# Kernel tuning notes

Measured on AMD Instinct MI355X. Metric: run time of the kernel, lower is better.

Reference implementation:

```python
import jax, jax.numpy as jnp
import numpy as np

NUM_TAGS = 32            # init arg
N = NUM_TAGS + 2         # internal num_tags (start/end appended)
START = N - 2
END = N - 1
B = 1024
T = 1024
NEG = -6969.0            # module's 'minus infinity' constant


def setup_inputs() -> dict:
    key = jax.random.key(0)
    k1, k2 = jax.random.split(key)
    features = jax.random.normal(k1, (B, T, N), dtype=jnp.float32)
    # learned parameter: transition matrix [N, N]
    transitions = jax.random.normal(k2, (N, N), dtype=jnp.float32)
    return {"features": features, "transitions": transitions}


def _viterbi(features, transitions):
    # features: [B, T, N]; transitions: [N, N]
    Bn, Tn, Nn = features.shape
    init = jnp.full((Bn, Nn), NEG, dtype=features.dtype).at[:, START].set(0.0)

    def step(scores, feat):
        # score[b, j, k] = scores[b, k] + feat[b, j] + transitions[j, k]
        sc = scores[:, None, :] + feat[:, :, None] + transitions[None, :, :]
        return jnp.max(sc, axis=-1), jnp.argmax(sc, axis=-1)

    feats_t = jnp.swapaxes(features, 0, 1)            # [T, B, N]
    scores, paths = jax.lax.scan(step, init, feats_t)  # paths: [T, B, N] int

    scores = scores + transitions[END]                # add transition to end tag
    best = jnp.max(scores, axis=-1)                   # [B]
    idx = jnp.argmax(scores, axis=-1)                 # [B]

    # backtrack through backpointers, from t = T-1 down to 0
    def back(i, path):
        ni = jnp.take_along_axis(path, i[:, None], axis=1)[:, 0]
        return ni, ni

    _, tags = jax.lax.scan(back, idx, paths, reverse=True)  # tags: [T, B]
    best_path = jnp.concatenate([tags.T, idx[:, None]], axis=1)  # [B, T+1]
    return best, best_path


def reference(features, transitions):
    return _viterbi(features, transitions)
```

## Files before the change

### kernel.cpp

```cpp
#include <hip/hip_runtime.h>
#include <stdint.h>

#define BB 1024
#define TT 1024
#define NN 34
#define NP 36
#define CH 9
#define NB 4
#define TPB (NB * NN * 4)
#define NEGV -6969.0f
#define PADV -1.0e30f

template<int C>
__device__ __forceinline__ int dpp_i(int x) {
    return __builtin_amdgcn_update_dpp(0, x, C, 0xF, 0xF, true);
}
template<int C>
__device__ __forceinline__ float dpp_f(float x) {
    return __int_as_float(dpp_i<C>(__float_as_int(x)));
}

__global__ __launch_bounds__(TPB) void viterbi_fwd(
        const float* __restrict__ feat,
        const float* __restrict__ trans,
        unsigned char* __restrict__ bp,
        float* __restrict__ sfin)
{
    __shared__ float s_lds[2][NB * NP];

    const int tid = threadIdx.x;
    const int bl  = tid / 136;
    const int r   = tid % 136;
    const int j   = r >> 2;
    const int h   = r & 3;
    const int bg  = blockIdx.x * NB + bl;
    const int k0  = h * CH;

    float tr[CH];
#pragma unroll
    for (int i = 0; i < CH; ++i) {
        int k = k0 + i;
        tr[i] = (k < NN) ? trans[j * NN + k] : 0.0f;
    }

    for (int e = tid; e < 2 * NB * NP; e += TPB) {
        int kk = e % NP;
        float v = (kk >= NN) ? PADV : ((kk == 32) ? 0.0f : NEGV);
        s_lds[0][0] = s_lds[0][0];
        ((float*)s_lds)[e] = v;
    }

    const float* fptr = feat + (size_t)bg * TT * NN + j;
    float f = fptr[0];

    unsigned char* bprow = bp + (size_t)bg * TT * NN + j;

    __syncthreads();

    int cur = 0;
    for (int t = 0; t < TT; ++t) {
        const float* sb = &s_lds[cur][bl * NP + k0];
        float sv[CH];
#pragma unroll
        for (int i = 0; i < CH; ++i) sv[i] = sb[i];

        float fn = fptr[(size_t)((t + 1 < TT) ? t + 1 : t) * NN];

        float m = -3.0e38f;
        int am = k0;
#pragma unroll
        for (int i = 0; i < CH; ++i) {
            float v = (sv[i] + f) + tr[i];
            bool gt = v > m;
            am = gt ? (k0 + i) : am;
            m  = gt ? v : m;
        }

        {
            float vo = dpp_f<0xB1>(m);
            int   ko = dpp_i<0xB1>(am);
            bool take = (vo > m) || (vo == m && ko < am);
            m  = take ? vo : m;
            am = take ? ko : am;
            vo = dpp_f<0x4E>(m);
            ko = dpp_i<0x4E>(am);
            take = (vo > m) || (vo == m && ko < am);
            m  = take ? vo : m;
            am = take ? ko : am;
        }

        int nxt = cur ^ 1;
        if (h == 0) {
            s_lds[nxt][bl * NP + j] = m;
            bprow[(size_t)t * NN] = (unsigned char)am;
        }
        f = fn;
        cur = nxt;
        __syncthreads();
    }

    if (h == 0) sfin[bg * NN + j] = s_lds[cur][bl * NP + j];
}

__global__ __launch_bounds__(TPB) void viterbi_btk(
        const unsigned char* __restrict__ bp,
        const float* __restrict__ sfin,
        const float* __restrict__ trans,
        float* __restrict__ out)
{
    __shared__ unsigned char bps[TT * NN];
    __shared__ float fsb[NN];
    __shared__ int   Fm[16][NN];
    __shared__ int   Eb[16];
    __shared__ int   idx_s;

    const int b = blockIdx.x;
    const int tid = threadIdx.x;

    {
        const uint4* src = (const uint4*)(bp + (size_t)b * (TT * NN));
        uint4* dst = (uint4*)bps;
        for (int i = tid; i < (TT * NN) / 16; i += TPB) dst[i] = src[i];
    }
    if (tid < NN) fsb[tid] = sfin[b * NN + tid] + trans[33 * NN + tid];
    __syncthreads();

    if (tid == 0) {
        float bm = fsb[0]; int bi = 0;
        for (int k = 1; k < NN; ++k) {
            if (fsb[k] > bm) { bm = fsb[k]; bi = k; }
        }
        out[b] = bm;
        idx_s = bi;
    }
    __syncthreads();

    const int c = tid / NN;
    const int x = tid % NN;

    {
        int m = x;
        for (int i = 63; i >= 0; --i) m = bps[(c * 64 + i) * NN + m];
        Fm[c][x] = m;
    }
    __syncthreads();

    if (tid == 0) {
        int e = idx_s;
        Eb[15] = e;
        for (int cc = 15; cc >= 1; --cc) { e = Fm[cc][e]; Eb[cc - 1] = e; }
    }
    __syncthreads();

    float* po = out + BB + (size_t)b * (TT + 1);
    if (x == Eb[c]) {
        int m = x;
        for (int i = 63; i >= 0; --i) {
            m = bps[(c * 64 + i) * NN + m];
            po[c * 64 + i] = (float)m;
        }
    }
    if (tid == 0) po[TT] = (float)idx_s;
}

extern "C" void kernel_launch(void* const* d_in, const int* in_sizes, int n_in,
                              void* d_out, int out_size, void* d_ws, size_t ws_size,
                              hipStream_t stream) {
    const float* feat  = (const float*)d_in[0];
    const float* trans = (const float*)d_in[1];
    float* out = (float*)d_out;

    unsigned char* bp = (unsigned char*)d_ws;
    float* sfin = (float*)((char*)d_ws + (size_t)BB * TT * NN);

    viterbi_fwd<<<BB / NB, TPB, 0, stream>>>(feat, trans, bp, sfin);
    viterbi_btk<<<BB, TPB, 0, stream>>>(bp, sfin, trans, out);
}
```

Measured before the change: 640.3 us.

## Fuse forward and backtrack into one kernel with lighter step and prefetch

Merges the forward recursion and the backtrack into a single kernel, so the separate launch and the sfin round trip go away. The backtrack now reads backpointers straight from global memory instead of staging them in LDS. Each step finds the max first and then the argmax by equality test, uses an lgkmcnt-only barrier, and prefetches features four steps ahead. Batches per block drop from 4 to 2 with an occupancy hint. The global backtrack reads are serial dependent loads and may have higher latency, though they likely hit in cache right after being written.

```diff
diff --git a/kernel.cpp b/kernel.cpp
--- a/kernel.cpp
+++ b/kernel.cpp
@@ -5,9 +5,8 @@
 #define TT 1024
 #define NN 34
 #define NP 36
-#define CH 9
-#define NB 4
-#define TPB (NB * NN * 4)
+#define NB 2
+#define TPB (NB * 136)
 #define NEGV -6969.0f
 #define PADV -1.0e30f
 
@@ -20,147 +19,133 @@
     return __int_as_float(dpp_i<C>(__float_as_int(x)));
 }
 
-__global__ __launch_bounds__(TPB) void viterbi_fwd(
+__device__ __forceinline__ void lds_barrier() {
+    asm volatile("s_waitcnt lgkmcnt(0)\n\ts_barrier" ::: "memory");
+}
+
+__global__ __launch_bounds__(TPB, 3) void viterbi_full(
         const float* __restrict__ feat,
         const float* __restrict__ trans,
-        unsigned char* __restrict__ bp,
-        float* __restrict__ sfin)
+        unsigned char* __restrict__ bpg,
+        float* __restrict__ out)
 {
-    __shared__ float s_lds[2][NB * NP];
+    __shared__ float sbuf[2][NB][NP];
+    __shared__ float fsb[NB][NN];
+    __shared__ unsigned char Fm[NB][16][NN];
+    __shared__ int Eb[NB][16];
+    __shared__ int idxs[NB];
 
     const int tid = threadIdx.x;
-    const int bl  = tid / 136;
-    const int r   = tid % 136;
+    const int bl  = (tid >= 136) ? 1 : 0;
+    const int r   = tid - bl * 136;
     const int j   = r >> 2;
     const int h   = r & 3;
+    const int k0  = h * 9;
     const int bg  = blockIdx.x * NB + bl;
-    const int k0  = h * CH;
-
-    float tr[CH];
-#pragma unroll
-    for (int i = 0; i < CH; ++i) {
-        int k = k0 + i;
-        tr[i] = (k < NN) ? trans[j * NN + k] : 0.0f;
-    }
 
     for (int e = tid; e < 2 * NB * NP; e += TPB) {
         int kk = e % NP;
-        float v = (kk >= NN) ? PADV : ((kk == 32) ? 0.0f : NEGV);
-        s_lds[0][0] = s_lds[0][0];
-        ((float*)s_lds)[e] = v;
+        ((float*)sbuf)[e] = (kk >= NN) ? PADV : ((kk == 32) ? 0.0f : NEGV);
     }
 
-    const float* fptr = feat + (size_t)bg * TT * NN + j;
-    float f = fptr[0];
+    float tr[9];
+    int   kreg[9];
+#pragma unroll
+    for (int i = 0; i < 9; ++i) {
+        int k = k0 + i;
+        tr[i]   = (k < NN) ? trans[j * NN + k] : 0.0f;
+        kreg[i] = k;
+    }
+    const float trE = (r < NN) ? trans[33 * NN + r] : 0.0f;
 
-    unsigned char* bprow = bp + (size_t)bg * TT * NN + j;
+    const float* fp = feat + (size_t)bg * TT * NN + j;
+    unsigned char* bpt = bpg + (size_t)bg * TT * NN + j;
+
+    float fr0 = fp[0 * NN], fr1 = fp[1 * NN], fr2 = fp[2 * NN], fr3 = fp[3 * NN];
+
+    float* const s0 = &sbuf[0][bl][0];
+    float* const s1 = &sbuf[1][bl][0];
 
     __syncthreads();
 
-    int cur = 0;
-    for (int t = 0; t < TT; ++t) {
-        const float* sb = &s_lds[cur][bl * NP + k0];
-        float sv[CH];
+    auto vstep = [&](const float* __restrict__ srd, float* __restrict__ swr,
+                     float fv, unsigned char* bpw) {
+        float vv[9];
 #pragma unroll
-        for (int i = 0; i < CH; ++i) sv[i] = sb[i];
+        for (int i = 0; i < 9; ++i) vv[i] = (srd[k0 + i] + fv) + tr[i];
+        float m = fmaxf(fmaxf(fmaxf(vv[0], vv[1]), fmaxf(vv[2], vv[3])),
+                        fmaxf(fmaxf(vv[4], vv[5]), fmaxf(vv[6], vv[7])));
+        m = fmaxf(m, vv[8]);
+        m = fmaxf(m, dpp_f<0xB1>(m));
+        m = fmaxf(m, dpp_f<0x4E>(m));
+        int am = 127;
+#pragma unroll
+        for (int i = 8; i >= 0; --i) am = (vv[i] == m) ? kreg[i] : am;
+        int ao = dpp_i<0xB1>(am); am = (ao < am) ? ao : am;
+        ao = dpp_i<0x4E>(am);     am = (ao < am) ? ao : am;
+        if (h == 0) { swr[j] = m; *bpw = (unsigned char)am; }
+        lds_barrier();
+    };
 
-        float fn = fptr[(size_t)((t + 1 < TT) ? t + 1 : t) * NN];
+    for (int n = 0; n < 255; ++n) {
+        { float f = fr0; fr0 = fp[4 * NN]; vstep(s0, s1, f, bpt + 0 * NN); }
+        { float f = fr1; fr1 = fp[5 * NN]; vstep(s1, s0, f, bpt + 1 * NN); }
+        { float f = fr2; fr2 = fp[6 * NN]; vstep(s0, s1, f, bpt + 2 * NN); }
+        { float f = fr3; fr3 = fp[7 * NN]; vstep(s1, s0, f, bpt + 3 * NN); }
+        fp += 4 * NN; bpt += 4 * NN;
+    }
+    vstep(s0, s1, fr0, bpt + 0 * NN);
+    vstep(s1, s0, fr1, bpt + 1 * NN);
+    vstep(s0, s1, fr2, bpt + 2 * NN);
+    vstep(s1, s0, fr3, bpt + 3 * NN);
 
-        float m = -3.0e38f;
-        int am = k0;
-#pragma unroll
-        for (int i = 0; i < CH; ++i) {
-            float v = (sv[i] + f) + tr[i];
-            bool gt = v > m;
-            am = gt ? (k0 + i) : am;
-            m  = gt ? v : m;
+    if (r < NN) fsb[bl][r] = s0[r] + trE;
+    __syncthreads();
+    if (r == 0) {
+        float bm = fsb[bl][0]; int bi = 0;
+        for (int k = 1; k < NN; ++k) {
+            float v = fsb[bl][k];
+            if (v > bm) { bm = v; bi = k; }
         }
-
-        {
-            float vo = dpp_f<0xB1>(m);
-            int   ko = dpp_i<0xB1>(am);
-            bool take = (vo > m) || (vo == m && ko < am);
-            m  = take ? vo : m;
-            am = take ? ko : am;
-            vo = dpp_f<0x4E>(m);
-            ko = dpp_i<0x4E>(am);
-            take = (vo > m) || (vo == m && ko < am);
-            m  = take ? vo : m;
-            am = take ? ko : am;
-        }
-
-        int nxt = cur ^ 1;
-        if (h == 0) {
-            s_lds[nxt][bl * NP + j] = m;
-            bprow[(size_t)t * NN] = (unsigned char)am;
-        }
-        f = fn;
-        cur = nxt;
-        __syncthreads();
-    }
-
-    if (h == 0) sfin[bg * NN + j] = s_lds[cur][bl * NP + j];
-}
-
-__global__ __launch_bounds__(TPB) void viterbi_btk(
-        const unsigned char* __restrict__ bp,
-        const float* __restrict__ sfin,
-        const float* __restrict__ trans,
-        float* __restrict__ out)
-{
-    __shared__ unsigned char bps[TT * NN];
-    __shared__ float fsb[NN];
-    __shared__ int   Fm[16][NN];
-    __shared__ int   Eb[16];
-    __shared__ int   idx_s;
-
-    const int b = blockIdx.x;
-    const int tid = threadIdx.x;
-
-    {
-        const uint4* src = (const uint4*)(bp + (size_t)b * (TT * NN));
-        uint4* dst = (uint4*)bps;
-        for (int i = tid; i < (TT * NN) / 16; i += TPB) dst[i] = src[i];
-    }
-    if (tid < NN) fsb[tid] = sfin[b * NN + tid] + trans[33 * NN + tid];
-    __syncthreads();
-
-    if (tid == 0) {
-        float bm = fsb[0]; int bi = 0;
-        for (int k = 1; k < NN; ++k) {
-            if (fsb[k] > bm) { bm = fsb[k]; bi = k; }
-        }
-        out[b] = bm;
-        idx_s = bi;
+        out[bg] = bm; idxs[bl] = bi;
     }
     __syncthreads();
 
-    const int c = tid / NN;
-    const int x = tid % NN;
+    const unsigned char* __restrict__ bb = bpg + (size_t)bg * TT * NN;
 
     {
-        int m = x;
-        for (int i = 63; i >= 0; --i) m = bps[(c * 64 + i) * NN + m];
-        Fm[c][x] = m;
+        int g = (r >= 102) ? 3 : ((r >= 68) ? 2 : ((r >= 34) ? 1 : 0));
+        int x = r - 34 * g;
+        int c0 = g, c1 = g + 4, c2 = g + 8, c3 = g + 12;
+        int m0 = x, m1 = x, m2 = x, m3 = x;
+        for (int i = 63; i >= 0; --i) {
+            m0 = bb[(size_t)((c0 * 64 + i) * NN) + m0];
+            m1 = bb[(size_t)((c1 * 64 + i) * NN) + m1];
+            m2 = bb[(size_t)((c2 * 64 + i) * NN) + m2];
+            m3 = bb[(size_t)((c3 * 64 + i) * NN) + m3];
+        }
+        Fm[bl][c0][x] = m0; Fm[bl][c1][x] = m1;
+        Fm[bl][c2][x] = m2; Fm[bl][c3][x] = m3;
     }
     __syncthreads();
 
-    if (tid == 0) {
-        int e = idx_s;
-        Eb[15] = e;
-        for (int cc = 15; cc >= 1; --cc) { e = Fm[cc][e]; Eb[cc - 1] = e; }
+    if (r == 0) {
+        int e = idxs[bl];
+        Eb[bl][15] = e;
+        for (int c = 15; c >= 1; --c) { e = Fm[bl][c][e]; Eb[bl][c - 1] = e; }
     }
     __syncthreads();
 
-    float* po = out + BB + (size_t)b * (TT + 1);
-    if (x == Eb[c]) {
-        int m = x;
+    float* po = out + BB + (size_t)bg * (TT + 1);
+    if (r < 16) {
+        int c = r;
+        int m = Eb[bl][c];
         for (int i = 63; i >= 0; --i) {
-            m = bps[(c * 64 + i) * NN + m];
+            m = bb[(size_t)((c * 64 + i) * NN) + m];
             po[c * 64 + i] = (float)m;
         }
     }
-    if (tid == 0) po[TT] = (float)idx_s;
+    if (r == 16) po[TT] = (float)idxs[bl];
 }
 
 extern "C" void kernel_launch(void* const* d_in, const int* in_sizes, int n_in,
@@ -169,10 +154,7 @@
     const float* feat  = (const float*)d_in[0];
     const float* trans = (const float*)d_in[1];
     float* out = (float*)d_out;
+    unsigned char* bp = (unsigned char*)d_ws;
 
-    unsigned char* bp = (unsigned char*)d_ws;
-    float* sfin = (float*)((char*)d_ws + (size_t)BB * TT * NN);
-
-    viterbi_fwd<<<BB / NB, TPB, 0, stream>>>(feat, trans, bp, sfin);
-    viterbi_btk<<<BB, TPB, 0, stream>>>(bp, sfin, trans, out);
+    viterbi_full<<<BB / NB, TPB, 0, stream>>>(feat, trans, bp, out);
 }
```

Result: faster. 547.5 us (-14.5%).
